# Kernel optimization log

Measured on AMD Instinct MI355X. Metric: run time of the kernel, lower is better.

## Reference

```python
import jax, jax.numpy as jnp
import numpy as np

N_NODES = 100000
N_EDGES = 1200000
N_GRAPHS = 1000
HID = 64
OUT = 4
ALPHA_FLAG = 0.03
NEG_SLOPE = 0.2


def _glorot(key, shape):
    fan_in, fan_out = shape[0], shape[-1]
    lim = (6.0 / (fan_in + fan_out)) ** 0.5
    return jax.random.uniform(key, shape, jnp.float32, -lim, lim)


def setup_inputs() -> dict:
    key = jax.random.key(0)
    ks = jax.random.split(key, 32)
    inp = {
        "x": jax.random.normal(ks[0], (N_NODES, 8), jnp.float32),
        "edge_index": jax.random.randint(ks[1], (2, N_EDGES), 0, N_NODES, jnp.int32),
        "batch": jnp.sort(jax.random.randint(ks[2], (N_NODES,), 0, N_GRAPHS, jnp.int32)),
        "climber": jax.random.normal(ks[3], (N_GRAPHS, 6), jnp.float32),
        # lin_in
        "W_in": _glorot(ks[4], (6, HID)), "b_in": jnp.zeros((HID,), jnp.float32),
        # climber_embed: LayerNorm(6) + Linear(6,64)
        "ln_g": jnp.ones((6,), jnp.float32), "ln_b": jnp.zeros((6,), jnp.float32),
        "W_c": _glorot(ks[5], (6, HID)), "b_c": jnp.zeros((HID,), jnp.float32),
        # film1 / film2: Linear(64,128)
        "Wf1": _glorot(ks[6], (HID, 2 * HID)), "bf1": jnp.zeros((2 * HID,), jnp.float32),
        "Wf2": _glorot(ks[7], (HID, 2 * HID)), "bf2": jnp.zeros((2 * HID,), jnp.float32),
        # GATConv 1 (heads=1): lin weight, att_src, att_dst, bias
        "Wg1": _glorot(ks[8], (HID, HID)), "as1": _glorot(ks[9], (HID, 1))[:, 0],
        "ad1": _glorot(ks[10], (HID, 1))[:, 0], "bg1": jnp.zeros((HID,), jnp.float32),
        # GATConv 2
        "Wg2": _glorot(ks[11], (HID, HID)), "as2": _glorot(ks[12], (HID, 1))[:, 0],
        "ad2": _glorot(ks[13], (HID, 1))[:, 0], "bg2": jnp.zeros((HID,), jnp.float32),
        # cls head
        "Wc1": _glorot(ks[14], (HID, HID)), "bc1": jnp.zeros((HID,), jnp.float32),
        "Wc2": _glorot(ks[15], (HID, OUT)), "bc2": jnp.zeros((OUT,), jnp.float32),
        # flag head
        "Wh1": _glorot(ks[16], (2, 8)), "bh1": jnp.zeros((8,), jnp.float32),
        "Wh2": _glorot(ks[17], (8, OUT)), "bh2": jnp.zeros((OUT,), jnp.float32),
    }
    return inp


def _gat(h, src, dst, W, a_src, a_dst, bias, n):
    # PyG GATConv, heads=1, concat=False, self-loops already appended.
    z = h @ W                                    # [N, H]
    e = jax.nn.leaky_relu((z @ a_src)[src] + (z @ a_dst)[dst], NEG_SLOPE)  # [E]
    m = jax.ops.segment_max(e, dst, num_segments=n)
    ex = jnp.exp(e - m[dst])
    s = jax.ops.segment_sum(ex, dst, num_segments=n)
    alpha = ex / (s[dst] + 1e-16)
    out = jax.ops.segment_sum(alpha[:, None] * z[src], dst, num_segments=n)
    return out + bias


def reference(x, edge_index, batch, climber, W_in, b_in, ln_g, ln_b, W_c, b_c,
              Wf1, bf1, Wf2, bf2, Wg1, as1, ad1, bg1, Wg2, as2, ad2, bg2,
              Wc1, bc1, Wc2, bc2, Wh1, bh1, Wh2, bh2):
    n = x.shape[0]
    # add self loops (PyG GATConv default)
    loop = jnp.arange(n, dtype=edge_index.dtype)
    src = jnp.concatenate([edge_index[0], loop])
    dst = jnp.concatenate([edge_index[1], loop])

    x_cont, flags = x[:, :6], x[:, 6:8]
    h = x_cont @ W_in + b_in

    # climber embed: LayerNorm + Linear + ReLU
    mu = jnp.mean(climber, -1, keepdims=True)
    var = jnp.var(climber, -1, keepdims=True)
    cn = (climber - mu) * jax.lax.rsqrt(var + 1e-5) * ln_g + ln_b
    c = jax.nn.relu(cn @ W_c + b_c)

    def film(h, Wf, bf):
        gb = c @ Wf + bf
        gamma, beta = jnp.split(gb, 2, axis=-1)
        return h * (1.0 + gamma[batch]) + beta[batch]

    h = film(h, Wf1, bf1)
    h = jax.nn.relu(_gat(h, src, dst, Wg1, as1, ad1, bg1, n))
    h = film(h, Wf2, bf2)
    h = jax.nn.relu(_gat(h, src, dst, Wg2, as2, ad2, bg2, n))

    # cls head (dropout inactive in eval)
    cls = jax.nn.relu(h @ Wc1 + bc1) @ Wc2 + bc2
    flag = jax.nn.relu(flags @ Wh1 + bh1) @ Wh2 + bh2
    return cls + ALPHA_FLAG * flag
```

## Files before the change

kernel.cpp:

```cpp
#include <hip/hip_runtime.h>
#include <math.h>

#define N_NODES 100000
#define N_EDGES 1200000
#define N_GRAPHS 1000
#define HID 64
#define NBUCK 256
#define NPB   391
#define BCAP  8192
#define EDGE_CHUNK 4096
#define S3_BLOCKS ((N_EDGES + EDGE_CHUNK - 1) / EDGE_CHUNK)
#define Z1_BLOCKS 98
#define LOG2E 1.4426950408889634f
#define N_TILES (N_NODES / 16)
#define AGG_BLOCKS (N_NODES / 16)

typedef _Float16 half_t;
typedef __attribute__((ext_vector_type(4))) _Float16 half4;
typedef __attribute__((ext_vector_type(8))) _Float16 half8;
typedef __attribute__((ext_vector_type(4))) float floatx4;

__global__ void k_climber_film(const float* __restrict__ climber,
                               const float* __restrict__ ln_g, const float* __restrict__ ln_b,
                               const float* __restrict__ W_c, const float* __restrict__ b_c,
                               const float* __restrict__ Wf1, const float* __restrict__ bf1,
                               const float* __restrict__ Wf2, const float* __restrict__ bf2,
                               const float* __restrict__ Wg2, const float* __restrict__ Wc1,
                               float* __restrict__ gb1, float* __restrict__ gb2,
                               half_t* __restrict__ Wp1, half_t* __restrict__ Wp2,
                               int* __restrict__ bucket_fill) {
    __shared__ float cl[64];
    int g = blockIdx.x;
    int j = threadIdx.x;
    if (g >= N_GRAPHS) {
        const float* Wsrc = (g == N_GRAPHS) ? Wg2 : Wc1;
        half_t*      Wdst = (g == N_GRAPHS) ? Wp1 : Wp2;
        for (int idx = j; idx < 4096; idx += 128) {
            int jj = idx & 7;
            int ko = (idx >> 3) & 1;
            int l  = (idx >> 4) & 63;
            int w  = idx >> 10;
            int c  = l & 15;
            int gg = l >> 4;
            Wdst[idx] = (half_t)Wsrc[(ko*32 + gg*8 + jj)*64 + c + 16*w];
        }
        return;
    }
    if (g == 0) {
        bucket_fill[j] = 0;
        bucket_fill[j + 128] = 0;
    }
    if (j < 64) {
        float v[6];
        float mu = 0.f;
        #pragma unroll
        for (int k = 0; k < 6; k++) { v[k] = climber[g*6+k]; mu += v[k]; }
        mu *= (1.f/6.f);
        float var = 0.f;
        #pragma unroll
        for (int k = 0; k < 6; k++) { float d = v[k]-mu; var += d*d; }
        var *= (1.f/6.f);
        float rs = rsqrtf(var + 1e-5f);
        float acc = b_c[j];
        #pragma unroll
        for (int k = 0; k < 6; k++) {
            float cn = (v[k]-mu)*rs*ln_g[k] + ln_b[k];
            acc += cn * W_c[k*64+j];
        }
        cl[j] = fmaxf(acc, 0.f);
    }
    __syncthreads();
    float a1 = bf1[j], a2 = bf2[j];
    #pragma unroll 8
    for (int k = 0; k < 64; k++) {
        float ck = cl[k];
        a1 += ck * Wf1[k*128+j];
        a2 += ck * Wf2[k*128+j];
    }
    gb1[g*128+j] = a1;
    gb2[g*128+j] = a2;
}

__global__ __launch_bounds__(1024) void k_bin(const int* __restrict__ ei,
                                              int* __restrict__ bucket_fill,
                                              int* __restrict__ staged) {
    __shared__ int hist[NBUCK];
    __shared__ int cursor[NBUCK];
    for (int t = threadIdx.x; t < NBUCK; t += blockDim.x) hist[t] = 0;
    __syncthreads();
    int e0 = blockIdx.x * EDGE_CHUNK;
    int e1 = min(e0 + EDGE_CHUNK, N_EDGES);
    for (int e = e0 + threadIdx.x; e < e1; e += blockDim.x)
        atomicAdd(&hist[ei[N_EDGES + e] / NPB], 1);
    __syncthreads();
    if (threadIdx.x < NBUCK) {
        int hv = hist[threadIdx.x];
        int start = threadIdx.x * BCAP;
        if (hv) start += atomicAdd(&bucket_fill[threadIdx.x], hv);
        cursor[threadIdx.x] = start;
    }
    __syncthreads();
    for (int e = e0 + threadIdx.x; e < e1; e += blockDim.x) {
        int src = ei[e], dst = ei[N_EDGES + e];
        int b = dst / NPB;
        int ldst = dst - b * NPB;
        int pos = atomicAdd(&cursor[b], 1);
        staged[pos] = (ldst << 17) | src;
    }
}

__global__ __launch_bounds__(1024) void k_mid(
        const int* __restrict__ staged, const int* __restrict__ bucket_fill,
        int* __restrict__ rowptr, int* __restrict__ csr_src,
        const float* __restrict__ x, const int* __restrict__ batch,
        const float* __restrict__ W_in, const float* __restrict__ b_in,
        const float* __restrict__ gb1, const float* __restrict__ W,
        const float* __restrict__ a_src, const float* __restrict__ a_dst,
        half_t* __restrict__ z, float* __restrict__ es, float* __restrict__ ed) {
    if (blockIdx.x < NBUCK) {
        __shared__ int bb[NBUCK];
        __shared__ int ldeg[NPB];
        __shared__ int sc[512];
        __shared__ int cursor[NPB];
        int b = blockIdx.x;
        if (threadIdx.x < NBUCK) bb[threadIdx.x] = bucket_fill[threadIdx.x];
        __syncthreads();
        for (int off = 1; off < NBUCK; off <<= 1) {
            int u = 0;
            if (threadIdx.x < NBUCK && threadIdx.x >= off) u = bb[threadIdx.x - off];
            __syncthreads();
            if (threadIdx.x < NBUCK) bb[threadIdx.x] += u;
            __syncthreads();
        }
        int bbase = (b == 0) ? 0 : bb[b-1];
        int bcnt  = bb[b] - bbase;
        const int* st = staged + b * BCAP;
        int n0 = b * NPB;
        int n1 = min(n0 + NPB, N_NODES);
        int nn = n1 - n0;
        for (int t = threadIdx.x; t < NPB; t += blockDim.x) ldeg[t] = 0;
        __syncthreads();
        for (int k = threadIdx.x; k < bcnt; k += blockDim.x)
            atomicAdd(&ldeg[st[k] >> 17], 1);
        __syncthreads();
        if (threadIdx.x < 512) sc[threadIdx.x] = (threadIdx.x < nn) ? ldeg[threadIdx.x] : 0;
        __syncthreads();
        for (int off = 1; off < 512; off <<= 1) {
            int u = 0;
            if (threadIdx.x < 512 && threadIdx.x >= off) u = sc[threadIdx.x - off];
            __syncthreads();
            if (threadIdx.x < 512) sc[threadIdx.x] += u;
            __syncthreads();
        }
        if (threadIdx.x < nn) {
            int pre = sc[threadIdx.x] - ldeg[threadIdx.x];
            rowptr[n0 + threadIdx.x] = bbase + pre;
            cursor[threadIdx.x] = bbase + pre;
        }
        if (b == 0 && threadIdx.x == 0) rowptr[N_NODES] = bb[NBUCK-1];
        __syncthreads();
        for (int k = threadIdx.x; k < bcnt; k += blockDim.x) {
            int v = st[k];
            int pos = atomicAdd(&cursor[v >> 17], 1);
            csr_src[pos] = v & 0x1FFFF;
        }
        return;
    }
    __shared__ float Wi[384];
    __shared__ float bi[64];
    __shared__ __align__(16) half_t zl[16][1024];
    for (int idx = threadIdx.x; idx < 384; idx += 1024) Wi[idx] = W_in[idx];
    if (threadIdx.x < 64) bi[threadIdx.x] = b_in[threadIdx.x];
    int wave = threadIdx.x >> 6;
    int l    = threadIdx.x & 63;
    int c    = l & 15;
    int g    = l >> 4;
    half8 Bf[2][4];
    #pragma unroll
    for (int ko = 0; ko < 2; ko++) {
        #pragma unroll
        for (int nt = 0; nt < 4; nt++) {
            half8 bvec;
            #pragma unroll
            for (int j = 0; j < 8; j++)
                bvec[j] = (half_t)W[(ko*32 + g*8 + j)*64 + c + 16*nt];
            Bf[ko][nt] = bvec;
        }
    }
    float as4[4], ad4[4];
    #pragma unroll
    for (int nt = 0; nt < 4; nt++) {
        as4[nt] = a_src[c + 16*nt] * LOG2E;
        ad4[nt] = a_dst[c + 16*nt] * LOG2E;
    }
    __syncthreads();
    int nWaves = Z1_BLOCKS * 16;
    int wid = (blockIdx.x - NBUCK) * 16 + wave;
    half_t* zw = zl[wave];
    for (int t = wid; t < N_TILES; t += nWaves) {
        int m0 = t * 16;
        int i = m0 + c;
        float xv[6];
        #pragma unroll
        for (int kk = 0; kk < 6; kk++) xv[kk] = x[i*8 + kk];
        int bg_ = batch[i];
        half8 A[2];
        #pragma unroll
        for (int s = 0; s < 2; s++) {
            int bk = s*32 + g*8;
            float acc[8];
            #pragma unroll
            for (int j = 0; j < 8; j++) acc[j] = bi[bk + j];
            #pragma unroll
            for (int kk = 0; kk < 6; kk++) {
                float xk = xv[kk];
                float4 w0 = *(const float4*)&Wi[kk*64 + bk];
                float4 w1 = *(const float4*)&Wi[kk*64 + bk + 4];
                acc[0] += xk*w0.x; acc[1] += xk*w0.y;
                acc[2] += xk*w0.z; acc[3] += xk*w0.w;
                acc[4] += xk*w1.x; acc[5] += xk*w1.y;
                acc[6] += xk*w1.z; acc[7] += xk*w1.w;
            }
            const float4* gbv = (const float4*)(gb1 + bg_*128);
            float4 ga0 = gbv[bk/4],      ga1 = gbv[bk/4 + 1];
            float4 be0 = gbv[16 + bk/4], be1 = gbv[16 + bk/4 + 1];
            half8 hv;
            hv[0] = (half_t)(acc[0]*(1.f+ga0.x) + be0.x);
            hv[1] = (half_t)(acc[1]*(1.f+ga0.y) + be0.y);
            hv[2] = (half_t)(acc[2]*(1.f+ga0.z) + be0.z);
            hv[3] = (half_t)(acc[3]*(1.f+ga0.w) + be0.w);
            hv[4] = (half_t)(acc[4]*(1.f+ga1.x) + be1.x);
            hv[5] = (half_t)(acc[5]*(1.f+ga1.y) + be1.y);
            hv[6] = (half_t)(acc[6]*(1.f+ga1.z) + be1.z);
            hv[7] = (half_t)(acc[7]*(1.f+ga1.w) + be1.w);
            A[s] = hv;
        }
        floatx4 D[4];
        #pragma unroll
        for (int nt = 0; nt < 4; nt++) {
            floatx4 acc = {0.f, 0.f, 0.f, 0.f};
            acc = __builtin_amdgcn_mfma_f32_16x16x32_f16(A[0], Bf[0][nt], acc, 0, 0, 0);
            acc = __builtin_amdgcn_mfma_f32_16x16x32_f16(A[1], Bf[1][nt], acc, 0, 0, 0);
            D[nt] = acc;
        }
        #pragma unroll
        for (int r = 0; r < 4; r++) {
            float ps = D[0][r]*as4[0] + D[1][r]*as4[1] + D[2][r]*as4[2] + D[3][r]*as4[3];
            float pd = D[0][r]*ad4[0] + D[1][r]*ad4[1] + D[2][r]*ad4[2] + D[3][r]*ad4[3];
            #pragma unroll
            for (int off = 1; off < 16; off <<= 1) {
                ps += __shfl_xor(ps, off, 16);
                pd += __shfl_xor(pd, off, 16);
            }
            if (c == 0) {
                es[m0 + g*4 + r] = ps;
                ed[m0 + g*4 + r] = pd;
            }
        }
        #pragma unroll
        for (int nt = 0; nt < 4; nt++) {
            #pragma unroll
            for (int r = 0; r < 4; r++)
                zw[(g*4 + r)*64 + c + 16*nt] = (half_t)D[nt][r];
        }
        __asm__ __volatile__("s_waitcnt lgkmcnt(0)" ::: "memory");
        const half8* zr = (const half8*)zw;
        half8 v0 = zr[l*2];
        half8 v1 = zr[l*2 + 1];
        half8* zo = (half8*)(z + (size_t)m0 * 64);
        zo[l*2]     = v0;
        zo[l*2 + 1] = v1;
        __asm__ __volatile__("s_waitcnt lgkmcnt(0)" ::: "memory");
    }
}

__device__ __forceinline__ float4 h4_to_f4(half4 h) {
    float4 f;
    f.x = (float)h.x; f.y = (float)h.y; f.z = (float)h.z; f.w = (float)h.w;
    return f;
}

template<int MODE>
__global__ __launch_bounds__(256) void k_agg_f(
        const int* __restrict__ rowptr, const int* __restrict__ csr_src,
        const float* __restrict__ es, const float* __restrict__ ed,
        const half_t* __restrict__ z, const float* __restrict__ bg,
        const int* __restrict__ batch, const float* __restrict__ gb,
        const half_t* __restrict__ Wp,
        const float* __restrict__ av_s, const float* __restrict__ av_d,
        half_t* __restrict__ zout, float* __restrict__ es_o, float* __restrict__ ed_o,
        const float* __restrict__ x,
        const float* __restrict__ bc1, const float* __restrict__ Wc2,
        const float* __restrict__ bc2,
        const float* __restrict__ Wh1, const float* __restrict__ bh1,
        const float* __restrict__ Wh2, const float* __restrict__ bh2,
        float* __restrict__ out) {
    __shared__ __align__(16) half_t h_l[1024];
    __shared__ __align__(16) half_t zl16[1024];
    __shared__ float red[4][16][4];
    int tidb = threadIdx.x;
    int il = tidb >> 4;
    int sl = tidb & 15;
    int m0 = blockIdx.x * 16;
    int i = m0 + il;

    int beg = rowptr[i], end = rowptr[i+1];
    int deg = end - beg;
    float edi = ed[i];
    float e_self = es[i] + edi;
    e_self = fmaxf(e_self, 0.2f * e_self);

    int svA = 0, svB = 0;
    float exA = 0.f, exB = 0.f;
    if (sl < deg) {
        svA = csr_src[beg + sl];
        float v = es[svA] + edi;
        exA = exp2f(fmaxf(v, 0.2f * v));
    }
    if (16 + sl < deg) {
        svB = csr_src[beg + 16 + sl];
        float v = es[svB] + edi;
        exB = exp2f(fmaxf(v, 0.2f * v));
    }
    float s = exA + exB;
    #pragma unroll
    for (int off = 1; off < 16; off <<= 1)
        s += __shfl_xor(s, off, 16);
    float ex = exp2f(e_self);
    s += ex;

    const half4* z4 = (const half4*)z;
    float4 zi = h4_to_f4(z4[i*16 + sl]);
    float4 acc = {ex*zi.x, ex*zi.y, ex*zi.z, ex*zi.w};

    int lim = (deg < 32) ? deg : 32;
    int k = 0;
    for (; k + 8 <= lim; k += 8) {
        int a[8]; float e[8];
        if (k < 16) {
            #pragma unroll
            for (int j = 0; j < 8; j++) {
                a[j] = __shfl(svA, k+j, 16);
                e[j] = __shfl(exA, k+j, 16);
            }
        } else {
            #pragma unroll
            for (int j = 0; j < 8; j++) {
                a[j] = __shfl(svB, k-16+j, 16);
                e[j] = __shfl(exB, k-16+j, 16);
            }
        }
        half4 q[8];
        #pragma unroll
        for (int j = 0; j < 8; j++) q[j] = z4[a[j]*16 + sl];
        #pragma unroll
        for (int j = 0; j < 8; j++) {
            float4 r = h4_to_f4(q[j]);
            acc.x += e[j]*r.x; acc.y += e[j]*r.y;
            acc.z += e[j]*r.z; acc.w += e[j]*r.w;
        }
    }
    for (; k + 4 <= lim; k += 4) {
        int a[4]; float e[4];
        if (k < 16) {
            #pragma unroll
            for (int j = 0; j < 4; j++) {
                a[j] = __shfl(svA, k+j, 16);
                e[j] = __shfl(exA, k+j, 16);
            }
        } else {
            #pragma unroll
            for (int j = 0; j < 4; j++) {
                a[j] = __shfl(svB, k-16+j, 16);
                e[j] = __shfl(exB, k-16+j, 16);
            }
        }
        half4 q[4];
        #pragma unroll
        for (int j = 0; j < 4; j++) q[j] = z4[a[j]*16 + sl];
        #pragma unroll
        for (int j = 0; j < 4; j++) {
            float4 r = h4_to_f4(q[j]);
            acc.x += e[j]*r.x; acc.y += e[j]*r.y;
            acc.z += e[j]*r.z; acc.w += e[j]*r.w;
        }
    }
    for (; k < lim; k++) {
        int a; float e2;
        if (k < 16) { a = __shfl(svA, k, 16);    e2 = __shfl(exA, k, 16); }
        else        { a = __shfl(svB, k-16, 16); e2 = __shfl(exB, k-16, 16); }
        float4 zr = h4_to_f4(z4[a*16 + sl]);
        acc.x += e2*zr.x; acc.y += e2*zr.y; acc.z += e2*zr.z; acc.w += e2*zr.w;
    }
    for (int kk = beg + 32; kk < end; kk++) {
        int sv = csr_src[kk];
        float v = es[sv] + edi;
        float e2 = exp2f(fmaxf(v, 0.2f * v));
        s += e2;
        float4 zr = h4_to_f4(z4[sv*16 + sl]);
        acc.x += e2*zr.x; acc.y += e2*zr.y; acc.z += e2*zr.z; acc.w += e2*zr.w;
    }
    float inv = 1.f / (s + 1e-16f);
    float4 bg4 = ((const float4*)bg)[sl];
    float4 o;
    o.x = fmaxf(acc.x*inv + bg4.x, 0.f);
    o.y = fmaxf(acc.y*inv + bg4.y, 0.f);
    o.z = fmaxf(acc.z*inv + bg4.z, 0.f);
    o.w = fmaxf(acc.w*inv + bg4.w, 0.f);
    if (MODE == 1) {
        int gidx = batch[i];
        const float4* gb4 = (const float4*)gb;
        float4 ga = gb4[gidx*32 + sl];
        float4 be = gb4[gidx*32 + 16 + sl];
        o.x = o.x*(1.f+ga.x) + be.x;
        o.y = o.y*(1.f+ga.y) + be.y;
        o.z = o.z*(1.f+ga.z) + be.z;
        o.w = o.w*(1.f+ga.w) + be.w;
    }
    half4 hv;
    hv.x = (half_t)o.x; hv.y = (half_t)o.y; hv.z = (half_t)o.z; hv.w = (half_t)o.w;
    *(half4*)((char*)h_l + il*128 + ((sl*8) ^ ((il & 7) << 4))) = hv;

    int l    = tidb & 63;
    int wave = tidb >> 6;
    int c    = l & 15;
    int g    = l >> 4;
    const half8* wp = (const half8*)(Wp + ((size_t)tidb << 4));
    half8 Bf0 = wp[0];
    half8 Bf1 = wp[1];
    float as_w = 0.f, ad_w = 0.f, bc1w = 0.f;
    float4 w2w = {0.f, 0.f, 0.f, 0.f};
    if (MODE == 1) {
        as_w = av_s[c + 16*wave] * LOG2E;
        ad_w = av_d[c + 16*wave] * LOG2E;
    } else {
        bc1w = bc1[c + 16*wave];
        w2w  = ((const float4*)Wc2)[c + 16*wave];
    }
    __syncthreads();
    half8 A0 = *(const half8*)((const char*)h_l + c*128 + ((g*16)      ^ ((c & 7) << 4)));
    half8 A1 = *(const half8*)((const char*)h_l + c*128 + ((64 + g*16) ^ ((c & 7) << 4)));
    floatx4 D = {0.f, 0.f, 0.f, 0.f};
    D = __builtin_amdgcn_mfma_f32_16x16x32_f16(A0, Bf0, D, 0, 0, 0);
    D = __builtin_amdgcn_mfma_f32_16x16x32_f16(A1, Bf1, D, 0, 0, 0);
    if (MODE == 1) {
        #pragma unroll
        for (int r = 0; r < 4; r++) {
            float ps = D[r]*as_w, pd = D[r]*ad_w;
            #pragma unroll
            for (int off = 1; off < 16; off <<= 1) {
                ps += __shfl_xor(ps, off, 16);
                pd += __shfl_xor(pd, off, 16);
            }
            if (c == 0) {
                red[wave][g*4 + r][0] = ps;
                red[wave][g*4 + r][1] = pd;
            }
            zl16[(g*4 + r)*64 + c + 16*wave] = (half_t)D[r];
        }
        __syncthreads();
        if (tidb < 16) {
            es_o[m0 + tidb] = red[0][tidb][0] + red[1][tidb][0] + red[2][tidb][0] + red[3][tidb][0];
            ed_o[m0 + tidb] = red[0][tidb][1] + red[1][tidb][1] + red[2][tidb][1] + red[3][tidb][1];
        }
        if (tidb < 128)
            ((half8*)(zout + (size_t)m0 * 64))[tidb] = ((const half8*)zl16)[tidb];
    } else {
        #pragma unroll
        for (int r = 0; r < 4; r++) {
            float tv = fmaxf(D[r] + bc1w, 0.f);
            float px = tv*w2w.x, py = tv*w2w.y, pz = tv*w2w.z, pw = tv*w2w.w;
            #pragma unroll
            for (int off = 1; off < 16; off <<= 1) {
                px += __shfl_xor(px, off, 16);
                py += __shfl_xor(py, off, 16);
                pz += __shfl_xor(pz, off, 16);
                pw += __shfl_xor(pw, off, 16);
            }
            if (c == 0) {
                red[wave][g*4 + r][0] = px;
                red[wave][g*4 + r][1] = py;
                red[wave][g*4 + r][2] = pz;
                red[wave][g*4 + r][3] = pw;
            }
        }
        __syncthreads();
        if (tidb < 16) {
            int m = m0 + tidb;
            float p0 = red[0][tidb][0] + red[1][tidb][0] + red[2][tidb][0] + red[3][tidb][0] + bc2[0];
            float p1 = red[0][tidb][1] + red[1][tidb][1] + red[2][tidb][1] + red[3][tidb][1] + bc2[1];
            float p2 = red[0][tidb][2] + red[1][tidb][2] + red[2][tidb][2] + red[3][tidb][2] + bc2[2];
            float p3 = red[0][tidb][3] + red[1][tidb][3] + red[2][tidb][3] + red[3][tidb][3] + bc2[3];
            float f0 = x[m*8+6], f1 = x[m*8+7];
            float t8[8];
            #pragma unroll
            for (int q = 0; q < 8; q++)
                t8[q] = fmaxf(f0*Wh1[q] + f1*Wh1[8+q] + bh1[q], 0.f);
            float fl[4];
            #pragma unroll
            for (int q = 0; q < 4; q++) {
                float a = bh2[q];
                #pragma unroll
                for (int rr = 0; rr < 8; rr++) a += t8[rr]*Wh2[rr*4+q];
                fl[q] = a;
            }
            float4 ov;
            ov.x = p0 + 0.03f*fl[0];
            ov.y = p1 + 0.03f*fl[1];
            ov.z = p2 + 0.03f*fl[2];
            ov.w = p3 + 0.03f*fl[3];
            ((float4*)out)[m] = ov;
        }
    }
}

extern "C" void kernel_launch(void* const* d_in, const int* in_sizes, int n_in,
                              void* d_out, int out_size, void* d_ws, size_t ws_size,
                              hipStream_t stream) {
    const float* x       = (const float*)d_in[0];
    const int*   ei      = (const int*)  d_in[1];
    const int*   batch   = (const int*)  d_in[2];
    const float* climber = (const float*)d_in[3];
    const float* W_in    = (const float*)d_in[4];
    const float* b_in    = (const float*)d_in[5];
    const float* ln_g    = (const float*)d_in[6];
    const float* ln_b    = (const float*)d_in[7];
    const float* W_c     = (const float*)d_in[8];
    const float* b_c     = (const float*)d_in[9];
    const float* Wf1     = (const float*)d_in[10];
    const float* bf1     = (const float*)d_in[11];
    const float* Wf2     = (const float*)d_in[12];
    const float* bf2     = (const float*)d_in[13];
    const float* Wg1     = (const float*)d_in[14];
    const float* as1     = (const float*)d_in[15];
    const float* ad1     = (const float*)d_in[16];
    const float* bg1     = (const float*)d_in[17];
    const float* Wg2     = (const float*)d_in[18];
    const float* as2     = (const float*)d_in[19];
    const float* ad2     = (const float*)d_in[20];
    const float* bg2     = (const float*)d_in[21];
    const float* Wc1     = (const float*)d_in[22];
    const float* bc1     = (const float*)d_in[23];
    const float* Wc2     = (const float*)d_in[24];
    const float* bc2     = (const float*)d_in[25];
    const float* Wh1     = (const float*)d_in[26];
    const float* bh1     = (const float*)d_in[27];
    const float* Wh2     = (const float*)d_in[28];
    const float* bh2     = (const float*)d_in[29];
    float* out = (float*)d_out;
    float* ws  = (float*)d_ws;

    float*  gb1         = ws;
    float*  gb2         = gb1 + 128000;
    half_t* Wp1         = (half_t*)(gb2 + 128000);
    half_t* Wp2         = Wp1 + 4096;
    half_t* zA          = Wp2 + 4096;
    half_t* zB          = zA + 6400000;
    float*  es1         = (float*)(zB + 6400000);
    float*  ed1         = es1 + N_NODES;
    float*  es2         = ed1 + N_NODES;
    float*  ed2         = es2 + N_NODES;
    int*    rowptr      = (int*)(ed2 + N_NODES);
    int*    csr_src     = rowptr + N_NODES + 1;
    int*    bucket_fill = csr_src + N_EDGES;
    int*    staged      = bucket_fill + NBUCK;

    k_climber_film<<<N_GRAPHS + 2, 128, 0, stream>>>(climber, ln_g, ln_b, W_c, b_c,
                                                     Wf1, bf1, Wf2, bf2, Wg2, Wc1,
                                                     gb1, gb2, Wp1, Wp2, bucket_fill);

    k_bin<<<S3_BLOCKS, 1024, 0, stream>>>(ei, bucket_fill, staged);

    k_mid<<<NBUCK + Z1_BLOCKS, 1024, 0, stream>>>(staged, bucket_fill, rowptr, csr_src,
                                                  x, batch, W_in, b_in, gb1, Wg1,
                                                  as1, ad1, zA, es1, ed1);

    k_agg_f<1><<<AGG_BLOCKS, 256, 0, stream>>>(rowptr, csr_src, es1, ed1, zA, bg1,
                                               batch, gb2, Wp1, as2, ad2,
                                               zB, es2, ed2,
                                               nullptr, nullptr, nullptr, nullptr,
                                               nullptr, nullptr, nullptr, nullptr,
                                               nullptr);

    k_agg_f<2><<<AGG_BLOCKS, 256, 0, stream>>>(rowptr, csr_src, es2, ed2, zB, bg2,
                                               batch, nullptr, Wp2, nullptr, nullptr,
                                               nullptr, nullptr, nullptr,
                                               x, bc1, Wc2, bc2, Wh1, bh1, Wh2, bh2,
                                               out);
}
```

Before: 251.4 us.

## Merge climber/FiLM and edge binning kernels, prefetch neighbor rows in aggregation

Folds the climber-embed/FiLM kernel and the edge-binning kernel into one launch, with eight graphs per 1024-thread block for the FiLM part. The bucket counters are now zeroed by a memset on the stream instead of inside the first kernel. The z-computation part of k_mid gets more blocks (98 to 256) and loads x with vector float4 reads. The aggregation kernel hoists the weight-fragment loads earlier and issues all 16 first-neighbor row gathers up front to overlap memory latency, at the cost of more registers.

```diff
diff --git a/kernel.cpp b/kernel.cpp
--- a/kernel.cpp
+++ b/kernel.cpp
@@ -10,7 +10,9 @@
 #define BCAP  8192
 #define EDGE_CHUNK 4096
 #define S3_BLOCKS ((N_EDGES + EDGE_CHUNK - 1) / EDGE_CHUNK)
-#define Z1_BLOCKS 98
+#define PRE_FILM_BLOCKS 125
+#define PRE_BIN0 127
+#define Z1_BLOCKS 256
 #define LOG2E 1.4426950408889634f
 #define N_TILES (N_NODES / 16)
 #define AGG_BLOCKS (N_NODES / 16)
@@ -20,22 +22,58 @@
 typedef __attribute__((ext_vector_type(8))) _Float16 half8;
 typedef __attribute__((ext_vector_type(4))) float floatx4;
 
-__global__ void k_climber_film(const float* __restrict__ climber,
-                               const float* __restrict__ ln_g, const float* __restrict__ ln_b,
-                               const float* __restrict__ W_c, const float* __restrict__ b_c,
-                               const float* __restrict__ Wf1, const float* __restrict__ bf1,
-                               const float* __restrict__ Wf2, const float* __restrict__ bf2,
-                               const float* __restrict__ Wg2, const float* __restrict__ Wc1,
-                               float* __restrict__ gb1, float* __restrict__ gb2,
-                               half_t* __restrict__ Wp1, half_t* __restrict__ Wp2,
-                               int* __restrict__ bucket_fill) {
-    __shared__ float cl[64];
-    int g = blockIdx.x;
-    int j = threadIdx.x;
-    if (g >= N_GRAPHS) {
-        const float* Wsrc = (g == N_GRAPHS) ? Wg2 : Wc1;
-        half_t*      Wdst = (g == N_GRAPHS) ? Wp1 : Wp2;
-        for (int idx = j; idx < 4096; idx += 128) {
+__global__ __launch_bounds__(1024) void k_pre(
+        const float* __restrict__ climber,
+        const float* __restrict__ ln_g, const float* __restrict__ ln_b,
+        const float* __restrict__ W_c, const float* __restrict__ b_c,
+        const float* __restrict__ Wf1, const float* __restrict__ bf1,
+        const float* __restrict__ Wf2, const float* __restrict__ bf2,
+        const float* __restrict__ Wg2, const float* __restrict__ Wc1,
+        float* __restrict__ gb1, float* __restrict__ gb2,
+        half_t* __restrict__ Wp1, half_t* __restrict__ Wp2,
+        const int* __restrict__ ei, int* __restrict__ bucket_fill,
+        int* __restrict__ staged) {
+    int bid = blockIdx.x;
+    if (bid < PRE_FILM_BLOCKS) {
+        __shared__ float cl[8][64];
+        int sub = threadIdx.x >> 7;
+        int j   = threadIdx.x & 127;
+        int g   = bid * 8 + sub;
+        if (j < 64) {
+            float v[6];
+            float mu = 0.f;
+            #pragma unroll
+            for (int k = 0; k < 6; k++) { v[k] = climber[g*6+k]; mu += v[k]; }
+            mu *= (1.f/6.f);
+            float var = 0.f;
+            #pragma unroll
+            for (int k = 0; k < 6; k++) { float d = v[k]-mu; var += d*d; }
+            var *= (1.f/6.f);
+            float rs = rsqrtf(var + 1e-5f);
+            float acc = b_c[j];
+            #pragma unroll
+            for (int k = 0; k < 6; k++) {
+                float cn = (v[k]-mu)*rs*ln_g[k] + ln_b[k];
+                acc += cn * W_c[k*64+j];
+            }
+            cl[sub][j] = fmaxf(acc, 0.f);
+        }
+        __syncthreads();
+        float a1 = bf1[j], a2 = bf2[j];
+        #pragma unroll 8
+        for (int k = 0; k < 64; k++) {
+            float ck = cl[sub][k];
+            a1 += ck * Wf1[k*128+j];
+            a2 += ck * Wf2[k*128+j];
+        }
+        gb1[g*128+j] = a1;
+        gb2[g*128+j] = a2;
+        return;
+    }
+    if (bid < PRE_BIN0) {
+        const float* Wsrc = (bid == PRE_FILM_BLOCKS) ? Wg2 : Wc1;
+        half_t*      Wdst = (bid == PRE_FILM_BLOCKS) ? Wp1 : Wp2;
+        for (int idx = threadIdx.x; idx < 4096; idx += 1024) {
             int jj = idx & 7;
             int ko = (idx >> 3) & 1;
             int l  = (idx >> 4) & 63;
@@ -46,49 +84,11 @@
         }
         return;
     }
-    if (g == 0) {
-        bucket_fill[j] = 0;
-        bucket_fill[j + 128] = 0;
-    }
-    if (j < 64) {
-        float v[6];
-        float mu = 0.f;
-        #pragma unroll
-        for (int k = 0; k < 6; k++) { v[k] = climber[g*6+k]; mu += v[k]; }
-        mu *= (1.f/6.f);
-        float var = 0.f;
-        #pragma unroll
-        for (int k = 0; k < 6; k++) { float d = v[k]-mu; var += d*d; }
-        var *= (1.f/6.f);
-        float rs = rsqrtf(var + 1e-5f);
-        float acc = b_c[j];
-        #pragma unroll
-        for (int k = 0; k < 6; k++) {
-            float cn = (v[k]-mu)*rs*ln_g[k] + ln_b[k];
-            acc += cn * W_c[k*64+j];
-        }
-        cl[j] = fmaxf(acc, 0.f);
-    }
-    __syncthreads();
-    float a1 = bf1[j], a2 = bf2[j];
-    #pragma unroll 8
-    for (int k = 0; k < 64; k++) {
-        float ck = cl[k];
-        a1 += ck * Wf1[k*128+j];
-        a2 += ck * Wf2[k*128+j];
-    }
-    gb1[g*128+j] = a1;
-    gb2[g*128+j] = a2;
-}
-
-__global__ __launch_bounds__(1024) void k_bin(const int* __restrict__ ei,
-                                              int* __restrict__ bucket_fill,
-                                              int* __restrict__ staged) {
     __shared__ int hist[NBUCK];
     __shared__ int cursor[NBUCK];
     for (int t = threadIdx.x; t < NBUCK; t += blockDim.x) hist[t] = 0;
     __syncthreads();
-    int e0 = blockIdx.x * EDGE_CHUNK;
+    int e0 = (bid - PRE_BIN0) * EDGE_CHUNK;
     int e1 = min(e0 + EDGE_CHUNK, N_EDGES);
     for (int e = e0 + threadIdx.x; e < e1; e += blockDim.x)
         atomicAdd(&hist[ei[N_EDGES + e] / NPB], 1);
@@ -197,12 +197,13 @@
     int nWaves = Z1_BLOCKS * 16;
     int wid = (blockIdx.x - NBUCK) * 16 + wave;
     half_t* zw = zl[wave];
+    const float4* x4p = (const float4*)x;
     for (int t = wid; t < N_TILES; t += nWaves) {
         int m0 = t * 16;
         int i = m0 + c;
-        float xv[6];
-        #pragma unroll
-        for (int kk = 0; kk < 6; kk++) xv[kk] = x[i*8 + kk];
+        float4 xa = x4p[i*2];
+        float4 xb = x4p[i*2 + 1];
+        float xv[6] = {xa.x, xa.y, xa.z, xa.w, xb.x, xb.y};
         int bg_ = batch[i];
         half8 A[2];
         #pragma unroll
@@ -304,24 +305,47 @@
     int m0 = blockIdx.x * 16;
     int i = m0 + il;
 
+    int l    = tidb & 63;
+    int wave = tidb >> 6;
+    int c    = l & 15;
+    int g    = l >> 4;
+    const half8* wp = (const half8*)(Wp + ((size_t)tidb << 4));
+    half8 Bf0 = wp[0];
+    half8 Bf1 = wp[1];
+    float as_w = 0.f, ad_w = 0.f, bc1w = 0.f;
+    float4 w2w = {0.f, 0.f, 0.f, 0.f};
+    if (MODE == 1) {
+        as_w = av_s[c + 16*wave] * LOG2E;
+        ad_w = av_d[c + 16*wave] * LOG2E;
+    } else {
+        bc1w = bc1[c + 16*wave];
+        w2w  = ((const float4*)Wc2)[c + 16*wave];
+    }
+
     int beg = rowptr[i], end = rowptr[i+1];
     int deg = end - beg;
     float edi = ed[i];
+
+    int svA = 0, svB = 0;
+    if (sl < deg)      svA = csr_src[beg + sl];
+    if (16 + sl < deg) svB = csr_src[beg + 16 + sl];
+
+    const half4* z4 = (const half4*)z;
+    int aP[16];
+    #pragma unroll
+    for (int j = 0; j < 16; j++) aP[j] = __shfl(svA, j, 16);
+    half4 qP[16];
+    #pragma unroll
+    for (int j = 0; j < 16; j++) qP[j] = z4[aP[j]*16 + sl];
+    float4 zi = h4_to_f4(z4[i*16 + sl]);
+    float esA = es[svA];
+    float esB = es[svB];
     float e_self = es[i] + edi;
     e_self = fmaxf(e_self, 0.2f * e_self);
-
-    int svA = 0, svB = 0;
-    float exA = 0.f, exB = 0.f;
-    if (sl < deg) {
-        svA = csr_src[beg + sl];
-        float v = es[svA] + edi;
-        exA = exp2f(fmaxf(v, 0.2f * v));
-    }
-    if (16 + sl < deg) {
-        svB = csr_src[beg + 16 + sl];
-        float v = es[svB] + edi;
-        exB = exp2f(fmaxf(v, 0.2f * v));
-    }
+    float vA = esA + edi, vB = esB + edi;
+    float exA = (sl < deg)      ? exp2f(fmaxf(vA, 0.2f * vA)) : 0.f;
+    float exB = (16 + sl < deg) ? exp2f(fmaxf(vB, 0.2f * vB)) : 0.f;
+
     float s = exA + exB;
     #pragma unroll
     for (int off = 1; off < 16; off <<= 1)
@@ -329,76 +353,67 @@
     float ex = exp2f(e_self);
     s += ex;
 
-    const half4* z4 = (const half4*)z;
-    float4 zi = h4_to_f4(z4[i*16 + sl]);
     float4 acc = {ex*zi.x, ex*zi.y, ex*zi.z, ex*zi.w};
 
-    int lim = (deg < 32) ? deg : 32;
-    int k = 0;
-    for (; k + 8 <= lim; k += 8) {
-        int a[8]; float e[8];
-        if (k < 16) {
-            #pragma unroll
-            for (int j = 0; j < 8; j++) {
-                a[j] = __shfl(svA, k+j, 16);
-                e[j] = __shfl(exA, k+j, 16);
-            }
-        } else {
+    #pragma unroll
+    for (int j = 0; j < 16; j++) {
+        float e = __shfl(exA, j, 16);
+        float4 r = h4_to_f4(qP[j]);
+        acc.x += e*r.x; acc.y += e*r.y;
+        acc.z += e*r.z; acc.w += e*r.w;
+    }
+
+    if (deg > 16) {
+        int lim = (deg < 32) ? deg : 32;
+        int k = 16;
+        for (; k + 8 <= lim; k += 8) {
+            int a[8]; float e[8];
             #pragma unroll
             for (int j = 0; j < 8; j++) {
                 a[j] = __shfl(svB, k-16+j, 16);
                 e[j] = __shfl(exB, k-16+j, 16);
             }
-        }
-        half4 q[8];
-        #pragma unroll
-        for (int j = 0; j < 8; j++) q[j] = z4[a[j]*16 + sl];
-        #pragma unroll
-        for (int j = 0; j < 8; j++) {
-            float4 r = h4_to_f4(q[j]);
-            acc.x += e[j]*r.x; acc.y += e[j]*r.y;
-            acc.z += e[j]*r.z; acc.w += e[j]*r.w;
-        }
-    }
-    for (; k + 4 <= lim; k += 4) {
-        int a[4]; float e[4];
-        if (k < 16) {
-            #pragma unroll
-            for (int j = 0; j < 4; j++) {
-                a[j] = __shfl(svA, k+j, 16);
-                e[j] = __shfl(exA, k+j, 16);
-            }
-        } else {
+            half4 q[8];
+            #pragma unroll
+            for (int j = 0; j < 8; j++) q[j] = z4[a[j]*16 + sl];
+            #pragma unroll
+            for (int j = 0; j < 8; j++) {
+                float4 r = h4_to_f4(q[j]);
+                acc.x += e[j]*r.x; acc.y += e[j]*r.y;
+                acc.z += e[j]*r.z; acc.w += e[j]*r.w;
+            }
+        }
+        for (; k + 4 <= lim; k += 4) {
+            int a[4]; float e[4];
             #pragma unroll
             for (int j = 0; j < 4; j++) {
                 a[j] = __shfl(svB, k-16+j, 16);
                 e[j] = __shfl(exB, k-16+j, 16);
             }
-        }
-        half4 q[4];
-        #pragma unroll
-        for (int j = 0; j < 4; j++) q[j] = z4[a[j]*16 + sl];
-        #pragma unroll
-        for (int j = 0; j < 4; j++) {
-            float4 r = h4_to_f4(q[j]);
-            acc.x += e[j]*r.x; acc.y += e[j]*r.y;
-            acc.z += e[j]*r.z; acc.w += e[j]*r.w;
-        }
-    }
-    for (; k < lim; k++) {
-        int a; float e2;
-        if (k < 16) { a = __shfl(svA, k, 16);    e2 = __shfl(exA, k, 16); }
-        else        { a = __shfl(svB, k-16, 16); e2 = __shfl(exB, k-16, 16); }
-        float4 zr = h4_to_f4(z4[a*16 + sl]);
-        acc.x += e2*zr.x; acc.y += e2*zr.y; acc.z += e2*zr.z; acc.w += e2*zr.w;
-    }
-    for (int kk = beg + 32; kk < end; kk++) {
-        int sv = csr_src[kk];
-        float v = es[sv] + edi;
-        float e2 = exp2f(fmaxf(v, 0.2f * v));
-        s += e2;
-        float4 zr = h4_to_f4(z4[sv*16 + sl]);
-        acc.x += e2*zr.x; acc.y += e2*zr.y; acc.z += e2*zr.z; acc.w += e2*zr.w;
+            half4 q[4];
+            #pragma unroll
+            for (int j = 0; j < 4; j++) q[j] = z4[a[j]*16 + sl];
+            #pragma unroll
+            for (int j = 0; j < 4; j++) {
+                float4 r = h4_to_f4(q[j]);
+                acc.x += e[j]*r.x; acc.y += e[j]*r.y;
+                acc.z += e[j]*r.z; acc.w += e[j]*r.w;
+            }
+        }
+        for (; k < lim; k++) {
+            int a = __shfl(svB, k-16, 16);
+            float e2 = __shfl(exB, k-16, 16);
+            float4 zr = h4_to_f4(z4[a*16 + sl]);
+            acc.x += e2*zr.x; acc.y += e2*zr.y; acc.z += e2*zr.z; acc.w += e2*zr.w;
+        }
+        for (int kk = beg + 32; kk < end; kk++) {
+            int sv = csr_src[kk];
+            float v = es[sv] + edi;
+            float e2 = exp2f(fmaxf(v, 0.2f * v));
+            s += e2;
+            float4 zr = h4_to_f4(z4[sv*16 + sl]);
+            acc.x += e2*zr.x; acc.y += e2*zr.y; acc.z += e2*zr.z; acc.w += e2*zr.w;
+        }
     }
     float inv = 1.f / (s + 1e-16f);
     float4 bg4 = ((const float4*)bg)[sl];
@@ -421,22 +436,6 @@
     hv.x = (half_t)o.x; hv.y = (half_t)o.y; hv.z = (half_t)o.z; hv.w = (half_t)o.w;
     *(half4*)((char*)h_l + il*128 + ((sl*8) ^ ((il & 7) << 4))) = hv;
 
-    int l    = tidb & 63;
-    int wave = tidb >> 6;
-    int c    = l & 15;
-    int g    = l >> 4;
-    const half8* wp = (const half8*)(Wp + ((size_t)tidb << 4));
-    half8 Bf0 = wp[0];
-    half8 Bf1 = wp[1];
-    float as_w = 0.f, ad_w = 0.f, bc1w = 0.f;
-    float4 w2w = {0.f, 0.f, 0.f, 0.f};
-    if (MODE == 1) {
-        as_w = av_s[c + 16*wave] * LOG2E;
-        ad_w = av_d[c + 16*wave] * LOG2E;
-    } else {
-        bc1w = bc1[c + 16*wave];
-        w2w  = ((const float4*)Wc2)[c + 16*wave];
-    }
     __syncthreads();
     half8 A0 = *(const half8*)((const char*)h_l + c*128 + ((g*16)      ^ ((c & 7) << 4)));
     half8 A1 = *(const half8*)((const char*)h_l + c*128 + ((64 + g*16) ^ ((c & 7) << 4)));
@@ -565,11 +564,12 @@
     int*    bucket_fill = csr_src + N_EDGES;
     int*    staged      = bucket_fill + NBUCK;
 
-    k_climber_film<<<N_GRAPHS + 2, 128, 0, stream>>>(climber, ln_g, ln_b, W_c, b_c,
+    hipMemsetAsync(bucket_fill, 0, NBUCK * sizeof(int), stream);
+
+    k_pre<<<PRE_BIN0 + S3_BLOCKS, 1024, 0, stream>>>(climber, ln_g, ln_b, W_c, b_c,
                                                      Wf1, bf1, Wf2, bf2, Wg2, Wc1,
-                                                     gb1, gb2, Wp1, Wp2, bucket_fill);
-
-    k_bin<<<S3_BLOCKS, 1024, 0, stream>>>(ei, bucket_fill, staged);
+                                                     gb1, gb2, Wp1, Wp2,
+                                                     ei, bucket_fill, staged);
 
     k_mid<<<NBUCK + Z1_BLOCKS, 1024, 0, stream>>>(staged, bucket_fill, rowptr, csr_src,
                                                   x, batch, W_in, b_in, gb1, Wg1,
```

Result: faster. 237.3 us (-5.6%).
